# Kernel optimization log

Hardware: AMD Instinct MI355X
Metric: run time of the kernel (lower is better)

## Reference

```python
import jax, jax.numpy as jnp
import numpy as np

HIDDEN = 128
N_LAYERS = 6
N_NODES = 50000
N_EDGES = 640000


def _glorot(key, shape):
    fan_in, fan_out = shape[0], shape[1]
    lim = (6.0 / (fan_in + fan_out)) ** 0.5
    return jax.random.uniform(key, shape, jnp.float32, -lim, lim)


def setup_inputs() -> dict:
    key = jax.random.key(0)
    ks = jax.random.split(key, 8)
    pos = jax.random.normal(ks[0], (N_NODES, 3), jnp.float32)
    edge_attr = jax.random.normal(ks[1], (N_EDGES, 3), jnp.float32)
    edge_index = jax.random.randint(ks[2], (2, N_EDGES), 0, N_NODES, jnp.int64)
    enc_w = _glorot(ks[3], (3, HIDDEN)); enc_b = jnp.zeros((HIDDEN,), jnp.float32)
    dec_w = _glorot(ks[4], (HIDDEN, 3)); dec_b = jnp.zeros((3,), jnp.float32)
    lk = jax.random.split(ks[5], 4 * N_LAYERS)
    edge_w1 = jnp.stack([_glorot(lk[4 * i + 0], (3 * HIDDEN, HIDDEN)) for i in range(N_LAYERS)])
    edge_w2 = jnp.stack([_glorot(lk[4 * i + 1], (HIDDEN, HIDDEN)) for i in range(N_LAYERS)])
    node_w1 = jnp.stack([_glorot(lk[4 * i + 2], (2 * HIDDEN, HIDDEN)) for i in range(N_LAYERS)])
    node_w2 = jnp.stack([_glorot(lk[4 * i + 3], (HIDDEN, HIDDEN)) for i in range(N_LAYERS)])
    edge_b1 = jnp.zeros((N_LAYERS, HIDDEN), jnp.float32)
    edge_b2 = jnp.zeros((N_LAYERS, HIDDEN), jnp.float32)
    node_b1 = jnp.zeros((N_LAYERS, HIDDEN), jnp.float32)
    node_b2 = jnp.zeros((N_LAYERS, HIDDEN), jnp.float32)
    return dict(pos=pos, edge_attr=edge_attr, edge_index=edge_index,
                enc_w=enc_w, enc_b=enc_b, dec_w=dec_w, dec_b=dec_b,
                edge_w1=edge_w1, edge_b1=edge_b1, edge_w2=edge_w2, edge_b2=edge_b2,
                node_w1=node_w1, node_b1=node_b1, node_w2=node_w2, node_b2=node_b2)


def _interaction(x, ef, src, dst, ew1, eb1, ew2, eb2, nw1, nb1, nw2, nb2, n_nodes):
    # message: concat(x_i=x[dst], x_j=x[src], edge_feature) -> edge MLP
    m = jnp.concatenate([x[dst], x[src], ef], axis=-1)            # [E, 3H]
    m = jax.nn.relu(m @ ew1 + eb1) @ ew2 + eb2                     # [E, H]
    # scatter-mean by target node
    sums = jax.ops.segment_sum(m, dst, num_segments=n_nodes)      # [N, H]
    cnt = jax.ops.segment_sum(jnp.ones((m.shape[0],), m.dtype), dst, num_segments=n_nodes)
    aggr = sums / jnp.maximum(cnt, 1.0)[:, None]
    node = jnp.concatenate([x, aggr], axis=-1)                     # [N, 2H]
    node = jax.nn.relu(node @ nw1 + nb1) @ nw2 + nb2               # [N, H]
    return x + node, ef + m


def reference(pos, edge_attr, edge_index, enc_w, enc_b, dec_w, dec_b,
              edge_w1, edge_b1, edge_w2, edge_b2,
              node_w1, node_b1, node_w2, node_b2):
    n_nodes = pos.shape[0]
    src = edge_index[0]
    dst = edge_index[1]
    x = jnp.zeros((n_nodes, HIDDEN), jnp.float32)
    ef = edge_attr @ enc_w + enc_b
    for i in range(N_LAYERS):
        x, ef = _interaction(x, ef, src, dst,
                             edge_w1[i], edge_b1[i], edge_w2[i], edge_b2[i],
                             node_w1[i], node_b1[i], node_w2[i], node_b2[i], n_nodes)
    out = x @ dec_w + dec_b                                        # [N, 3]
    # F.normalize(dim=1, eps=1e-12)
    norm = jnp.linalg.norm(out, axis=1, keepdims=True)
    return out / jnp.maximum(norm, 1e-12)
```

## Files before the change

kernel.cpp:

```cpp
#include <hip/hip_runtime.h>
#include <cstdint>

#define HIDDEN  128
#define NLAYERS 6
#define NNODES  50000
#define NEDGES  640000

typedef short short8 __attribute__((ext_vector_type(8)));
typedef float f32x4  __attribute__((ext_vector_type(4)));
typedef unsigned int   u32x4 __attribute__((ext_vector_type(4)));
typedef unsigned short u16x4 __attribute__((ext_vector_type(4)));

__device__ __forceinline__ float bf2f(unsigned short u) {
    return __uint_as_float(((unsigned int)u) << 16);
}
__device__ __forceinline__ unsigned short f2bf(float f) {
    unsigned int u = __float_as_uint(f);
    unsigned int r = u + 0x7FFFu + ((u >> 16) & 1u);
    return (unsigned short)(r >> 16);
}
__device__ __forceinline__ unsigned int pack2(float a, float b) {
    unsigned int r;
    asm("v_cvt_pk_bf16_f32 %0, %1, %2" : "=v"(r) : "v"(a), "v"(b));
    return r;
}
__device__ __forceinline__ void unpack8u(u32x4 v, float* f) {
    f[0] = bf2f((unsigned short)(v.x & 0xffff)); f[1] = bf2f((unsigned short)(v.x >> 16));
    f[2] = bf2f((unsigned short)(v.y & 0xffff)); f[3] = bf2f((unsigned short)(v.y >> 16));
    f[4] = bf2f((unsigned short)(v.z & 0xffff)); f[5] = bf2f((unsigned short)(v.z >> 16));
    f[6] = bf2f((unsigned short)(v.w & 0xffff)); f[7] = bf2f((unsigned short)(v.w >> 16));
}

__device__ __forceinline__ void barrier_lgkm() {
    asm volatile("s_waitcnt lgkmcnt(0)" ::: "memory");
    __builtin_amdgcn_s_barrier();
    __builtin_amdgcn_sched_barrier(0);
}

__global__ void detect_kernel(const int* __restrict__ ei, int* __restrict__ flag)
{
    int lane = threadIdx.x;
    int v = ei[2 * lane + 1];
    unsigned long long b = __ballot(v != 0);
    if (lane == 0) *flag = (b != 0ULL) ? 1 : 0;
}

__global__ void normidx_kernel(const int* __restrict__ ei, const int* __restrict__ flag,
                               int* __restrict__ s32, int* __restrict__ d32)
{
    int e = blockIdx.x * blockDim.x + threadIdx.x;
    if (e >= NEDGES) return;
    int s, d;
    if (*flag) { s = ei[e]; d = ei[NEDGES + e]; }
    else       { s = ei[2 * e]; d = ei[2 * (NEDGES + e)]; }
    s32[e] = min(max(s, 0), NNODES - 1);
    d32[e] = min(max(d, 0), NNODES - 1);
}

__global__ void degree_kernel(const int* __restrict__ dst, int* __restrict__ deg)
{
    int e = blockIdx.x * blockDim.x + threadIdx.x;
    if (e < NEDGES) atomicAdd(&deg[dst[e]], 1);
}

#define SCAN_T 1024
__global__ void scan_kernel(const int* __restrict__ deg, int* __restrict__ off,
                            int* __restrict__ cursor)
{
    __shared__ int part[SCAN_T];
    const int t = threadIdx.x;
    const int CH = (NNODES + SCAN_T - 1) / SCAN_T;
    const int base = t * CH;
    int s = 0;
    for (int i = 0; i < CH; ++i) {
        int idx = base + i;
        if (idx < NNODES) s += deg[idx];
    }
    part[t] = s;
    __syncthreads();
    for (int d = 1; d < SCAN_T; d <<= 1) {
        int v = (t >= d) ? part[t - d] : 0;
        __syncthreads();
        part[t] += v;
        __syncthreads();
    }
    int run = (t == 0) ? 0 : part[t - 1];
    for (int i = 0; i < CH; ++i) {
        int idx = base + i;
        if (idx < NNODES) {
            off[idx] = run;
            cursor[idx] = run;
            run += deg[idx];
        }
    }
    if (t == SCAN_T - 1) off[NNODES] = run;
}

__global__ void scatter_kernel(const int* __restrict__ s32, const int* __restrict__ d32,
                               int* __restrict__ cursor,
                               int* __restrict__ sp, int* __restrict__ dp, int* __restrict__ ep)
{
    int e = blockIdx.x * blockDim.x + threadIdx.x;
    if (e >= NEDGES) return;
    int d = d32[e];
    int p = atomicAdd(&cursor[d], 1);
    sp[p] = s32[e];
    dp[p] = d;
    ep[p] = e;
}

__global__ void transpose_kernel(const float* __restrict__ W, unsigned short* __restrict__ WT,
                                 int K, int N, int L)
{
    long idx = (long)blockIdx.x * 256 + threadIdx.x;
    long tot = (long)L * K * N;
    if (idx >= tot) return;
    int kn = (int)(idx % ((long)K * N));
    int l  = (int)(idx / ((long)K * N));
    int k = kn / N;
    int n = kn % N;
    WT[(long)l * K * N + (long)n * K + k] = f2bf(W[idx]);
}

__global__ void encode_kernel(const float* __restrict__ ea,
                              const float* __restrict__ w,
                              const float* __restrict__ b,
                              const int* __restrict__ ep,
                              unsigned short* __restrict__ ef)
{
    int idx = blockIdx.x * blockDim.x + threadIdx.x;
    int p = idx >> 5;
    if (p >= NEDGES) return;
    int e = ep[p];
    int j = (idx & 31) << 2;
    float a0 = ea[e * 3 + 0], a1 = ea[e * 3 + 1], a2 = ea[e * 3 + 2];
    float4 w0 = *(const float4*)(w + 0 * HIDDEN + j);
    float4 w1 = *(const float4*)(w + 1 * HIDDEN + j);
    float4 w2 = *(const float4*)(w + 2 * HIDDEN + j);
    float4 bb = *(const float4*)(b + j);
    ushort4 o;
    o.x = f2bf(fmaf(a0, w0.x, fmaf(a1, w1.x, fmaf(a2, w2.x, bb.x))));
    o.y = f2bf(fmaf(a0, w0.y, fmaf(a1, w1.y, fmaf(a2, w2.y, bb.y))));
    o.z = f2bf(fmaf(a0, w0.z, fmaf(a1, w1.z, fmaf(a2, w2.z, bb.z))));
    o.w = f2bf(fmaf(a0, w0.w, fmaf(a1, w1.w, fmaf(a2, w2.w, bb.w))));
    *(ushort4*)(ef + (long)p * HIDDEN + j) = o;
}

__global__ __launch_bounds__(256, 3)
void edge_layer_mfma(const unsigned short* __restrict__ Xa,
                     const unsigned short* __restrict__ Xb,
                     unsigned short* __restrict__ ef,
                     float* __restrict__ sums,
                     const int* __restrict__ sp,
                     const int* __restrict__ dp,
                     const unsigned short* __restrict__ W1T,
                     const float* __restrict__ b1,
                     const unsigned short* __restrict__ W2T,
                     const float* __restrict__ b2)
{
    __shared__ __align__(16) unsigned char buf[45056];
    unsigned short* Hs = (unsigned short*)buf;
    unsigned short* Bs = (unsigned short*)(buf + 34816);
    __shared__ int dv[128];
    __shared__ int sv[128];

    const int tid = threadIdx.x;
    const int nwg = (int)gridDim.x;
    const int bid = (int)blockIdx.x;
    const int sb  = (bid & 7) * (nwg >> 3) + (bid >> 3);
    const long eb = (long)sb * 128;

    if (tid < 128) dv[tid]       = dp[eb + tid];
    else           sv[tid - 128] = sp[eb + tid - 128];

    const int lane = tid & 63;
    const int wv   = tid >> 6;
    const int mn   = lane & 15;
    const int q    = lane >> 4;
    const int bn   = tid >> 1;
    const int bk   = (tid & 1) << 4;

    u32x4 pw0, pw1;
    {
        const unsigned short* wp = W1T + (long)bn * 384 + 256 + bk;
        pw0 = *(const u32x4*)wp;
        pw1 = *(const u32x4*)(wp + 8);
    }

    short8 efold0[4], efold1[4];
    {
        const unsigned short* a0 = ef + (eb + wv * 32 + mn) * HIDDEN + (q << 3);
        const unsigned short* a1 = a0 + 16 * HIDDEN;
#pragma unroll
        for (int c = 0; c < 4; ++c) {
            efold0[c] = *(const short8*)(a0 + (c << 5));
            efold1[c] = *(const short8*)(a1 + (c << 5));
        }
    }

    f32x4 acc[2][8];
#pragma unroll
    for (int h = 0; h < 2; ++h)
#pragma unroll
        for (int t = 0; t < 8; ++t) acc[h][t] = (f32x4)0.0f;

    for (int c = 0; c < 4; ++c) {
        *(u32x4*)&Bs[bn * 40 + bk]     = pw0;
        *(u32x4*)&Bs[bn * 40 + bk + 8] = pw1;
        barrier_lgkm();
        if (c + 1 < 4) {
            const unsigned short* wp = W1T + (long)bn * 384 + 256 + ((c + 1) << 5) + bk;
            pw0 = *(const u32x4*)wp;
            pw1 = *(const u32x4*)(wp + 8);
        }
        short8 af0 = efold0[c];
        short8 af1 = efold1[c];
#pragma unroll
        for (int nt = 0; nt < 8; ++nt) {
            short8 bf = *(short8*)&Bs[(nt * 16 + mn) * 40 + (q << 3)];
            acc[0][nt] = __builtin_amdgcn_mfma_f32_16x16x32_bf16(af0, bf, acc[0][nt], 0, 0, 0);
            acc[1][nt] = __builtin_amdgcn_mfma_f32_16x16x32_bf16(af1, bf, acc[1][nt], 0, 0, 0);
        }
        barrier_lgkm();
    }

#pragma unroll
    for (int h = 0; h < 2; ++h)
#pragma unroll
        for (int nt = 0; nt < 8; ++nt)
#pragma unroll
            for (int r = 0; r < 4; r += 2) {
                unsigned int p = pack2(acc[h][nt][r], acc[h][nt][r + 1]);
                Hs[(wv * 32 + h * 16 + q * 4 + r)     * 136 + nt * 16 + mn] = (unsigned short)p;
                Hs[(wv * 32 + h * 16 + q * 4 + r + 1) * 136 + nt * 16 + mn] = (unsigned short)(p >> 16);
            }

    {
        const int row  = wv * 32 + (lane >> 1);
        const int ch   = (lane & 1) << 6;
        const unsigned short* xap = Xa + (long)dv[row] * HIDDEN + ch;
        const unsigned short* xbp = Xb + (long)sv[row] * HIDDEN + ch;
        unsigned short* hp = &Hs[row * 136 + ch];
#pragma unroll
        for (int i = 0; i < 8; ++i) {
            u32x4 va = *(const u32x4*)(xap + (i << 3));
            u32x4 vb = *(const u32x4*)(xbp + (i << 3));
            u32x4 vp = *(u32x4*)(hp + (i << 3));
            float fa[8], fb[8], fp[8];
            unpack8u(va, fa); unpack8u(vb, fb); unpack8u(vp, fp);
            const float* bp = b1 + ch + (i << 3);
            u32x4 nw;
            float h0 = fmaxf(fp[0] + fa[0] + fb[0] + bp[0], 0.0f);
            float h1 = fmaxf(fp[1] + fa[1] + fb[1] + bp[1], 0.0f);
            float h2 = fmaxf(fp[2] + fa[2] + fb[2] + bp[2], 0.0f);
            float h3 = fmaxf(fp[3] + fa[3] + fb[3] + bp[3], 0.0f);
            float h4 = fmaxf(fp[4] + fa[4] + fb[4] + bp[4], 0.0f);
            float h5 = fmaxf(fp[5] + fa[5] + fb[5] + bp[5], 0.0f);
            float h6 = fmaxf(fp[6] + fa[6] + fb[6] + bp[6], 0.0f);
            float h7 = fmaxf(fp[7] + fa[7] + fb[7] + bp[7], 0.0f);
            nw.x = pack2(h0, h1); nw.y = pack2(h2, h3);
            nw.z = pack2(h4, h5); nw.w = pack2(h6, h7);
            *(u32x4*)(hp + (i << 3)) = nw;
        }
    }

    f32x4 acc2[2][8];
#pragma unroll
    for (int h = 0; h < 2; ++h)
#pragma unroll
        for (int t = 0; t < 8; ++t) acc2[h][t] = (f32x4)0.0f;
    {
        const unsigned short* wp = W2T + (long)bn * 128 + bk;
        pw0 = *(const u32x4*)wp;
        pw1 = *(const u32x4*)(wp + 8);
    }
    for (int c = 0; c < 4; ++c) {
        *(u32x4*)&Bs[bn * 40 + bk]     = pw0;
        *(u32x4*)&Bs[bn * 40 + bk + 8] = pw1;
        barrier_lgkm();
        if (c + 1 < 4) {
            const unsigned short* wp = W2T + (long)bn * 128 + ((c + 1) << 5) + bk;
            pw0 = *(const u32x4*)wp;
            pw1 = *(const u32x4*)(wp + 8);
        }
        short8 af0 = *(short8*)&Hs[(wv * 32 + mn) * 136 + (c << 5) + (q << 3)];
        short8 af1 = *(short8*)&Hs[(wv * 32 + 16 + mn) * 136 + (c << 5) + (q << 3)];
#pragma unroll
        for (int nt = 0; nt < 8; ++nt) {
            short8 bf = *(short8*)&Bs[(nt * 16 + mn) * 40 + (q << 3)];
            acc2[0][nt] = __builtin_amdgcn_mfma_f32_16x16x32_bf16(af0, bf, acc2[0][nt], 0, 0, 0);
            acc2[1][nt] = __builtin_amdgcn_mfma_f32_16x16x32_bf16(af1, bf, acc2[1][nt], 0, 0, 0);
        }
        barrier_lgkm();
    }

#pragma unroll
    for (int h = 0; h < 2; ++h)
#pragma unroll
        for (int nt = 0; nt < 8; ++nt) {
            float b2v = b2[nt * 16 + mn];
#pragma unroll
            for (int r = 0; r < 4; r += 2) {
                unsigned int p = pack2(acc2[h][nt][r] + b2v, acc2[h][nt][r + 1] + b2v);
                Hs[(wv * 32 + h * 16 + q * 4 + r)     * 136 + nt * 16 + mn] = (unsigned short)p;
                Hs[(wv * 32 + h * 16 + q * 4 + r + 1) * 136 + nt * 16 + mn] = (unsigned short)(p >> 16);
            }
        }

#pragma unroll
    for (int h = 0; h < 2; ++h) {
        const int row = wv * 32 + h * 16 + mn;
        unsigned short* ep_ = ef + (eb + row) * HIDDEN + (q << 3);
#pragma unroll
        for (int c = 0; c < 4; ++c) {
            u32x4 mh = *(u32x4*)&Hs[row * 136 + (c << 5) + (q << 3)];
            float m[8], e[8];
            unpack8u(mh, m);
            short8 eo = h ? efold1[c] : efold0[c];
            u32x4 eu = *(u32x4*)&eo;
            unpack8u(eu, e);
            u32x4 nw;
            nw.x = pack2(e[0] + m[0], e[1] + m[1]);
            nw.y = pack2(e[2] + m[2], e[3] + m[3]);
            nw.z = pack2(e[4] + m[4], e[5] + m[5]);
            nw.w = pack2(e[6] + m[6], e[7] + m[7]);
            *(u32x4*)(ep_ + (c << 5)) = nw;
        }
    }

    {
        const int cp = (tid & 63) << 1;
        const int qr = tid >> 6;
        float s0 = 0.0f, s1 = 0.0f;
        int cur = dv[qr * 32];
        for (int r = 0; r < 32; ++r) {
            const int row = qr * 32 + r;
            const int d = dv[row];
            if (d != cur) {
                atomicAdd(&sums[(long)cur * HIDDEN + cp], s0);
                atomicAdd(&sums[(long)cur * HIDDEN + cp + 1], s1);
                s0 = 0.0f; s1 = 0.0f;
                cur = d;
            }
            unsigned int u = *(unsigned int*)&Hs[row * 136 + cp];
            s0 += bf2f((unsigned short)(u & 0xffff));
            s1 += bf2f((unsigned short)(u >> 16));
        }
        atomicAdd(&sums[(long)cur * HIDDEN + cp], s0);
        atomicAdd(&sums[(long)cur * HIDDEN + cp + 1], s1);
    }
}

__global__ __launch_bounds__(256, 5)
void node_layer_mfma(float* __restrict__ x,
                     float* __restrict__ sums,
                     const int* __restrict__ deg,
                     const unsigned short* __restrict__ N1T,
                     const float* __restrict__ b1,
                     const unsigned short* __restrict__ N2T,
                     const float* __restrict__ b2,
                     const unsigned short* __restrict__ W1Tn,
                     unsigned short* __restrict__ Xa,
                     unsigned short* __restrict__ Xb)
{
    __shared__ __align__(16) unsigned char nbuf[27648];
    unsigned short* Hs = (unsigned short*)nbuf;
    unsigned short* Bs = (unsigned short*)(nbuf + 17408);

    const int tid = threadIdx.x;
    const long n0 = (long)blockIdx.x * 64;

    const int lane = tid & 63;
    const int wv   = tid >> 6;
    const int mn   = lane & 15;
    const int q    = lane >> 4;
    const int srow = tid >> 2;
    const int sseg = tid & 3;
    const int bn   = tid >> 1;
    const int bk   = (tid & 1) << 4;

    long arow = n0 + wv * 16 + mn;
    if (arow >= NNODES) arow = NNODES - 1;
    const float* xr = x + arow * HIDDEN;
    const float* sr = sums + arow * HIDDEN;
    const float cv = 1.0f / fmaxf((float)deg[arow], 1.0f);

    f32x4 acc[8];
#pragma unroll
    for (int t = 0; t < 8; ++t) acc[t] = (f32x4)0.0f;

    float4 pa0, pa1;
    u32x4 pb0, pb1;
    {
        const unsigned short* wp = N1T + (long)bn * 256 + bk;
        pb0 = *(const u32x4*)wp;
        pb1 = *(const u32x4*)(wp + 8);
        const float* ap = xr + (q << 3);
        pa0 = *(const float4*)ap;
        pa1 = *(const float4*)(ap + 4);
    }
    float scCur = 1.0f;
    for (int c = 0; c < 8; ++c) {
        short8 af;
        {
            unsigned int* au = (unsigned int*)&af;
            au[0] = pack2(pa0.x * scCur, pa0.y * scCur);
            au[1] = pack2(pa0.z * scCur, pa0.w * scCur);
            au[2] = pack2(pa1.x * scCur, pa1.y * scCur);
            au[3] = pack2(pa1.z * scCur, pa1.w * scCur);
        }
        *(u32x4*)&Bs[bn * 40 + bk]     = pb0;
        *(u32x4*)&Bs[bn * 40 + bk + 8] = pb1;
        barrier_lgkm();
        if (c + 1 < 8) {
            const int cn = c + 1;
            const float* base = (cn < 4) ? xr : sr;
            scCur = (cn < 4) ? 1.0f : cv;
            const float* ap = base + ((cn & 3) << 5) + (q << 3);
            pa0 = *(const float4*)ap;
            pa1 = *(const float4*)(ap + 4);
            const unsigned short* wp = N1T + (long)bn * 256 + (cn << 5) + bk;
            pb0 = *(const u32x4*)wp;
            pb1 = *(const u32x4*)(wp + 8);
        }
#pragma unroll
        for (int nt = 0; nt < 8; ++nt) {
            short8 bf = *(short8*)&Bs[(nt * 16 + mn) * 40 + (q << 3)];
            acc[nt] = __builtin_amdgcn_mfma_f32_16x16x32_bf16(af, bf, acc[nt], 0, 0, 0);
        }
        barrier_lgkm();
    }

    {
        long row = n0 + srow;
        if (row < NNODES) {
            float4 z = make_float4(0.f, 0.f, 0.f, 0.f);
            float* p = sums + row * HIDDEN + (sseg << 5);
#pragma unroll
            for (int i = 0; i < 8; ++i) ((float4*)p)[i] = z;
        }
    }

#pragma unroll
    for (int nt = 0; nt < 8; ++nt) {
        float b1v = b1[nt * 16 + mn];
#pragma unroll
        for (int r = 0; r < 4; r += 2) {
            float h0 = fmaxf(acc[nt][r]     + b1v, 0.0f);
            float h1 = fmaxf(acc[nt][r + 1] + b1v, 0.0f);
            unsigned int p = pack2(h0, h1);
            Hs[(wv * 16 + q * 4 + r)     * 136 + nt * 16 + mn] = (unsigned short)p;
            Hs[(wv * 16 + q * 4 + r + 1) * 136 + nt * 16 + mn] = (unsigned short)(p >> 16);
        }
    }

    f32x4 acc2[8];
#pragma unroll
    for (int t = 0; t < 8; ++t) acc2[t] = (f32x4)0.0f;
    {
        const unsigned short* wp = N2T + (long)bn * 128 + bk;
        pb0 = *(const u32x4*)wp;
        pb1 = *(const u32x4*)(wp + 8);
    }
    for (int c = 0; c < 4; ++c) {
        *(u32x4*)&Bs[bn * 40 + bk]     = pb0;
        *(u32x4*)&Bs[bn * 40 + bk + 8] = pb1;
        barrier_lgkm();
        if (c + 1 < 4) {
            const unsigned short* wp = N2T + (long)bn * 128 + ((c + 1) << 5) + bk;
            pb0 = *(const u32x4*)wp;
            pb1 = *(const u32x4*)(wp + 8);
        }
        short8 af = *(short8*)&Hs[(wv * 16 + mn) * 136 + (c << 5) + (q << 3)];
#pragma unroll
        for (int nt = 0; nt < 8; ++nt) {
            short8 bf = *(short8*)&Bs[(nt * 16 + mn) * 40 + (q << 3)];
            acc2[nt] = __builtin_amdgcn_mfma_f32_16x16x32_bf16(af, bf, acc2[nt], 0, 0, 0);
        }
        barrier_lgkm();
    }

#pragma unroll
    for (int nt = 0; nt < 8; ++nt) {
        float b2v = b2[nt * 16 + mn];
        float xns[4];
#pragma unroll
        for (int r = 0; r < 4; ++r) {
            long row = n0 + wv * 16 + q * 4 + r;
            float xn = 0.0f;
            if (row < NNODES) {
                float* p = x + row * HIDDEN + nt * 16 + mn;
                xn = *p + acc2[nt][r] + b2v;
                *p = xn;
            }
            xns[r] = xn;
        }
        unsigned int p0 = pack2(xns[0], xns[1]);
        unsigned int p1 = pack2(xns[2], xns[3]);
        Hs[(wv * 16 + q * 4 + 0) * 136 + nt * 16 + mn] = (unsigned short)p0;
        Hs[(wv * 16 + q * 4 + 1) * 136 + nt * 16 + mn] = (unsigned short)(p0 >> 16);
        Hs[(wv * 16 + q * 4 + 2) * 136 + nt * 16 + mn] = (unsigned short)p1;
        Hs[(wv * 16 + q * 4 + 3) * 136 + nt * 16 + mn] = (unsigned short)(p1 >> 16);
    }

    if (W1Tn) {
#pragma unroll
        for (int half = 0; half < 2; ++half) {
            f32x4 accN[8];
#pragma unroll
            for (int t = 0; t < 8; ++t) accN[t] = (f32x4)0.0f;
            const int kbase = half << 7;
            {
                const unsigned short* wp = W1Tn + (long)bn * 384 + kbase + bk;
                pb0 = *(const u32x4*)wp;
                pb1 = *(const u32x4*)(wp + 8);
            }
            for (int c = 0; c < 4; ++c) {
                *(u32x4*)&Bs[bn * 40 + bk]     = pb0;
                *(u32x4*)&Bs[bn * 40 + bk + 8] = pb1;
                barrier_lgkm();
                if (c + 1 < 4) {
                    const unsigned short* wp = W1Tn + (long)bn * 384 + kbase + ((c + 1) << 5) + bk;
                    pb0 = *(const u32x4*)wp;
                    pb1 = *(const u32x4*)(wp + 8);
                }
                short8 af = *(short8*)&Hs[(wv * 16 + mn) * 136 + (c << 5) + (q << 3)];
#pragma unroll
                for (int nt = 0; nt < 8; ++nt) {
                    short8 bf = *(short8*)&Bs[(nt * 16 + mn) * 40 + (q << 3)];
                    accN[nt] = __builtin_amdgcn_mfma_f32_16x16x32_bf16(af, bf, accN[nt], 0, 0, 0);
                }
                barrier_lgkm();
            }
            unsigned short* Xout = half ? Xb : Xa;
#pragma unroll
            for (int nt = 0; nt < 8; ++nt) {
#pragma unroll
                for (int r = 0; r < 4; r += 2) {
                    unsigned int p = pack2(accN[nt][r], accN[nt][r + 1]);
                    long row0 = n0 + wv * 16 + q * 4 + r;
                    if (row0 < NNODES)
                        Xout[row0 * HIDDEN + nt * 16 + mn] = (unsigned short)p;
                    if (row0 + 1 < NNODES)
                        Xout[(row0 + 1) * HIDDEN + nt * 16 + mn] = (unsigned short)(p >> 16);
                }
            }
        }
    }
}

__global__ void decode_kernel(const float* __restrict__ x,
                              const float* __restrict__ w,
                              const float* __restrict__ b,
                              float* __restrict__ out)
{
    int gid = blockIdx.x * blockDim.x + threadIdx.x;
    int node = gid >> 6;
    int lane = threadIdx.x & 63;
    if (node >= NNODES) return;
    float a0 = 0.f, a1 = 0.f, a2 = 0.f;
#pragma unroll
    for (int k = lane; k < HIDDEN; k += 64) {
        float xv = x[(long)node * HIDDEN + k];
        a0 = fmaf(xv, w[k * 3 + 0], a0);
        a1 = fmaf(xv, w[k * 3 + 1], a1);
        a2 = fmaf(xv, w[k * 3 + 2], a2);
    }
#pragma unroll
    for (int off = 32; off > 0; off >>= 1) {
        a0 += __shfl_down(a0, off);
        a1 += __shfl_down(a1, off);
        a2 += __shfl_down(a2, off);
    }
    if (lane == 0) {
        a0 += b[0]; a1 += b[1]; a2 += b[2];
        float nrm = sqrtf(a0 * a0 + a1 * a1 + a2 * a2);
        float inv = 1.0f / fmaxf(nrm, 1e-12f);
        out[(long)node * 3 + 0] = a0 * inv;
        out[(long)node * 3 + 1] = a1 * inv;
        out[(long)node * 3 + 2] = a2 * inv;
    }
}

extern "C" void kernel_launch(void* const* d_in, const int* in_sizes, int n_in,
                              void* d_out, int out_size, void* d_ws, size_t ws_size,
                              hipStream_t stream)
{
    const float* edge_attr = (const float*)d_in[1];
    const int*   ei        = (const int*)d_in[2];
    const float* enc_w     = (const float*)d_in[3];
    const float* enc_b     = (const float*)d_in[4];
    const float* dec_w     = (const float*)d_in[5];
    const float* dec_b     = (const float*)d_in[6];
    const float* edge_w1   = (const float*)d_in[7];
    const float* edge_b1   = (const float*)d_in[8];
    const float* edge_w2   = (const float*)d_in[9];
    const float* edge_b2   = (const float*)d_in[10];
    const float* node_w1   = (const float*)d_in[11];
    const float* node_b1   = (const float*)d_in[12];
    const float* node_w2   = (const float*)d_in[13];
    const float* node_b2   = (const float*)d_in[14];

    char* ws = (char*)d_ws;
    unsigned short* ef  = (unsigned short*)(ws);
    float* x      = (float*)(ws + 163840000L);
    float* sums   = (float*)(ws + 189440000L);
    int*   src32  = (int*)  (ws + 215040000L);
    int*   dst32  = (int*)  (ws + 217600000L);
    int*   sp     = (int*)  (ws + 220160000L);
    int*   dp     = (int*)  (ws + 222720000L);
    int*   eperm  = (int*)  (ws + 225280000L);
    int*   deg    = (int*)  (ws + 227840000L);
    int*   off    = (int*)  (ws + 228040704L);
    int*   cursor = (int*)  (ws + 228241408L);
    int*   flag   = (int*)  (ws + 228442112L);
    unsigned short* W1T = (unsigned short*)(ws + 228442176L);
    unsigned short* W2T = (unsigned short*)(ws + 229032000L);
    unsigned short* N1T = (unsigned short*)(ws + 229228608L);
    unsigned short* N2T = (unsigned short*)(ws + 229621824L);
    unsigned short* Xa  = (unsigned short*)(ws + 229818432L);
    unsigned short* Xb  = (unsigned short*)(ws + 242618432L);

    float* out = (float*)d_out;

    hipMemsetAsync(x, 0, (size_t)NNODES * HIDDEN * sizeof(float), stream);
    hipMemsetAsync(sums, 0, (size_t)NNODES * HIDDEN * sizeof(float), stream);
    hipMemsetAsync(deg, 0, 200704, stream);
    hipMemsetAsync(Xa, 0, 25600000, stream);

    detect_kernel<<<1, 64, 0, stream>>>(ei, flag);
    normidx_kernel<<<(NEDGES + 255) / 256, 256, 0, stream>>>(ei, flag, src32, dst32);
    degree_kernel<<<(NEDGES + 255) / 256, 256, 0, stream>>>(dst32, deg);
    scan_kernel<<<1, SCAN_T, 0, stream>>>(deg, off, cursor);
    scatter_kernel<<<(NEDGES + 255) / 256, 256, 0, stream>>>(src32, dst32, cursor, sp, dp, eperm);
    encode_kernel<<<(NEDGES * 32 + 255) / 256, 256, 0, stream>>>(edge_attr, enc_w, enc_b, eperm, ef);

    transpose_kernel<<<(6 * 384 * 128 + 255) / 256, 256, 0, stream>>>(edge_w1, W1T, 384, 128, 6);
    transpose_kernel<<<(6 * 128 * 128 + 255) / 256, 256, 0, stream>>>(edge_w2, W2T, 128, 128, 6);
    transpose_kernel<<<(6 * 256 * 128 + 255) / 256, 256, 0, stream>>>(node_w1, N1T, 256, 128, 6);
    transpose_kernel<<<(6 * 128 * 128 + 255) / 256, 256, 0, stream>>>(node_w2, N2T, 128, 128, 6);

    for (int l = 0; l < NLAYERS; ++l) {
        edge_layer_mfma<<<NEDGES / 128, 256, 0, stream>>>(
            Xa, Xb, ef, sums, sp, dp,
            W1T + (long)l * 384 * 128, edge_b1 + (long)l * HIDDEN,
            W2T + (long)l * 128 * 128, edge_b2 + (long)l * HIDDEN);
        const unsigned short* w1next = (l + 1 < NLAYERS) ? (W1T + (long)(l + 1) * 384 * 128) : nullptr;
        node_layer_mfma<<<(NNODES + 63) / 64, 256, 0, stream>>>(
            x, sums, deg,
            N1T + (long)l * 256 * 128, node_b1 + (long)l * HIDDEN,
            N2T + (long)l * 128 * 128, node_b2 + (long)l * HIDDEN,
            w1next, Xa, Xb);
    }

    decode_kernel<<<(NNODES * 64 + 255) / 256, 256, 0, stream>>>(x, dec_w, dec_b, out);
}
```

Measured before the change: 1.546 ms.

## Split edge-layer work across 8 waves of 16 rows instead of 4 waves of 32

The edge layer kernel now launches 512 threads per block, and each wave handles 16 edge rows instead of 32. Per-thread accumulators are halved, weight staging uses one 16-byte load per thread, and the gather, epilogue and segmented atomic reduction are remapped to match. The aim is to cut register pressure and raise occupancy so there are more waves to hide gather latency. In exchange, the shared weight tile is reused by half as many MFMA rows per wave, and the segmented sums flush atomics more often because each run covers only 16 rows.

```diff
diff --git a/kernel.cpp b/kernel.cpp
--- a/kernel.cpp
+++ b/kernel.cpp
@@ -9,7 +9,6 @@
 typedef short short8 __attribute__((ext_vector_type(8)));
 typedef float f32x4  __attribute__((ext_vector_type(4)));
 typedef unsigned int   u32x4 __attribute__((ext_vector_type(4)));
-typedef unsigned short u16x4 __attribute__((ext_vector_type(4)));
 
 __device__ __forceinline__ float bf2f(unsigned short u) {
     return __uint_as_float(((unsigned int)u) << 16);
@@ -146,7 +145,7 @@
     *(ushort4*)(ef + (long)p * HIDDEN + j) = o;
 }
 
-__global__ __launch_bounds__(256, 3)
+__global__ __launch_bounds__(512, 6)
 void edge_layer_mfma(const unsigned short* __restrict__ Xa,
                      const unsigned short* __restrict__ Xb,
                      unsigned short* __restrict__ ef,
@@ -170,79 +169,66 @@
     const int sb  = (bid & 7) * (nwg >> 3) + (bid >> 3);
     const long eb = (long)sb * 128;
 
-    if (tid < 128) dv[tid]       = dp[eb + tid];
-    else           sv[tid - 128] = sp[eb + tid - 128];
+    if (tid < 128)      dv[tid]       = dp[eb + tid];
+    else if (tid < 256) sv[tid - 128] = sp[eb + tid - 128];
 
     const int lane = tid & 63;
     const int wv   = tid >> 6;
     const int mn   = lane & 15;
     const int q    = lane >> 4;
-    const int bn   = tid >> 1;
-    const int bk   = (tid & 1) << 4;
-
-    u32x4 pw0, pw1;
+    const int bn   = tid >> 2;
+    const int bk   = (tid & 3) << 3;
+
+    u32x4 pw0;
     {
         const unsigned short* wp = W1T + (long)bn * 384 + 256 + bk;
         pw0 = *(const u32x4*)wp;
-        pw1 = *(const u32x4*)(wp + 8);
-    }
-
-    short8 efold0[4], efold1[4];
-    {
-        const unsigned short* a0 = ef + (eb + wv * 32 + mn) * HIDDEN + (q << 3);
-        const unsigned short* a1 = a0 + 16 * HIDDEN;
-#pragma unroll
-        for (int c = 0; c < 4; ++c) {
-            efold0[c] = *(const short8*)(a0 + (c << 5));
-            efold1[c] = *(const short8*)(a1 + (c << 5));
-        }
-    }
-
-    f32x4 acc[2][8];
-#pragma unroll
-    for (int h = 0; h < 2; ++h)
-#pragma unroll
-        for (int t = 0; t < 8; ++t) acc[h][t] = (f32x4)0.0f;
+    }
+
+    short8 efold[4];
+    {
+        const unsigned short* a0 = ef + (eb + wv * 16 + mn) * HIDDEN + (q << 3);
+#pragma unroll
+        for (int c = 0; c < 4; ++c) efold[c] = *(const short8*)(a0 + (c << 5));
+    }
+
+    f32x4 acc[8];
+#pragma unroll
+    for (int t = 0; t < 8; ++t) acc[t] = (f32x4)0.0f;
 
     for (int c = 0; c < 4; ++c) {
-        *(u32x4*)&Bs[bn * 40 + bk]     = pw0;
-        *(u32x4*)&Bs[bn * 40 + bk + 8] = pw1;
+        *(u32x4*)&Bs[bn * 40 + bk] = pw0;
         barrier_lgkm();
         if (c + 1 < 4) {
             const unsigned short* wp = W1T + (long)bn * 384 + 256 + ((c + 1) << 5) + bk;
             pw0 = *(const u32x4*)wp;
-            pw1 = *(const u32x4*)(wp + 8);
-        }
-        short8 af0 = efold0[c];
-        short8 af1 = efold1[c];
+        }
+        short8 af = efold[c];
 #pragma unroll
         for (int nt = 0; nt < 8; ++nt) {
             short8 bf = *(short8*)&Bs[(nt * 16 + mn) * 40 + (q << 3)];
-            acc[0][nt] = __builtin_amdgcn_mfma_f32_16x16x32_bf16(af0, bf, acc[0][nt], 0, 0, 0);
-            acc[1][nt] = __builtin_amdgcn_mfma_f32_16x16x32_bf16(af1, bf, acc[1][nt], 0, 0, 0);
-        }
-        barrier_lgkm();
-    }
-
-#pragma unroll
-    for (int h = 0; h < 2; ++h)
-#pragma unroll
-        for (int nt = 0; nt < 8; ++nt)
-#pragma unroll
-            for (int r = 0; r < 4; r += 2) {
-                unsigned int p = pack2(acc[h][nt][r], acc[h][nt][r + 1]);
-                Hs[(wv * 32 + h * 16 + q * 4 + r)     * 136 + nt * 16 + mn] = (unsigned short)p;
-                Hs[(wv * 32 + h * 16 + q * 4 + r + 1) * 136 + nt * 16 + mn] = (unsigned short)(p >> 16);
-            }
-
-    {
-        const int row  = wv * 32 + (lane >> 1);
-        const int ch   = (lane & 1) << 6;
+            acc[nt] = __builtin_amdgcn_mfma_f32_16x16x32_bf16(af, bf, acc[nt], 0, 0, 0);
+        }
+        barrier_lgkm();
+    }
+
+#pragma unroll
+    for (int nt = 0; nt < 8; ++nt)
+#pragma unroll
+        for (int r = 0; r < 4; r += 2) {
+            unsigned int p = pack2(acc[nt][r], acc[nt][r + 1]);
+            Hs[(wv * 16 + q * 4 + r)     * 136 + nt * 16 + mn] = (unsigned short)p;
+            Hs[(wv * 16 + q * 4 + r + 1) * 136 + nt * 16 + mn] = (unsigned short)(p >> 16);
+        }
+
+    {
+        const int row = wv * 16 + (lane >> 2);
+        const int ch  = (lane & 3) << 5;
         const unsigned short* xap = Xa + (long)dv[row] * HIDDEN + ch;
         const unsigned short* xbp = Xb + (long)sv[row] * HIDDEN + ch;
         unsigned short* hp = &Hs[row * 136 + ch];
 #pragma unroll
-        for (int i = 0; i < 8; ++i) {
+        for (int i = 0; i < 4; ++i) {
             u32x4 va = *(const u32x4*)(xap + (i << 3));
             u32x4 vb = *(const u32x4*)(xbp + (i << 3));
             u32x4 vp = *(u32x4*)(hp + (i << 3));
@@ -264,60 +250,49 @@
         }
     }
 
-    f32x4 acc2[2][8];
-#pragma unroll
-    for (int h = 0; h < 2; ++h)
-#pragma unroll
-        for (int t = 0; t < 8; ++t) acc2[h][t] = (f32x4)0.0f;
+    f32x4 acc2[8];
+#pragma unroll
+    for (int t = 0; t < 8; ++t) acc2[t] = (f32x4)0.0f;
     {
         const unsigned short* wp = W2T + (long)bn * 128 + bk;
         pw0 = *(const u32x4*)wp;
-        pw1 = *(const u32x4*)(wp + 8);
     }
     for (int c = 0; c < 4; ++c) {
-        *(u32x4*)&Bs[bn * 40 + bk]     = pw0;
-        *(u32x4*)&Bs[bn * 40 + bk + 8] = pw1;
+        *(u32x4*)&Bs[bn * 40 + bk] = pw0;
         barrier_lgkm();
         if (c + 1 < 4) {
             const unsigned short* wp = W2T + (long)bn * 128 + ((c + 1) << 5) + bk;
             pw0 = *(const u32x4*)wp;
-            pw1 = *(const u32x4*)(wp + 8);
-        }
-        short8 af0 = *(short8*)&Hs[(wv * 32 + mn) * 136 + (c << 5) + (q << 3)];
-        short8 af1 = *(short8*)&Hs[(wv * 32 + 16 + mn) * 136 + (c << 5) + (q << 3)];
+        }
+        short8 af = *(short8*)&Hs[(wv * 16 + mn) * 136 + (c << 5) + (q << 3)];
 #pragma unroll
         for (int nt = 0; nt < 8; ++nt) {
             short8 bf = *(short8*)&Bs[(nt * 16 + mn) * 40 + (q << 3)];
-            acc2[0][nt] = __builtin_amdgcn_mfma_f32_16x16x32_bf16(af0, bf, acc2[0][nt], 0, 0, 0);
-            acc2[1][nt] = __builtin_amdgcn_mfma_f32_16x16x32_bf16(af1, bf, acc2[1][nt], 0, 0, 0);
-        }
-        barrier_lgkm();
-    }
-
-#pragma unroll
-    for (int h = 0; h < 2; ++h)
-#pragma unroll
-        for (int nt = 0; nt < 8; ++nt) {
-            float b2v = b2[nt * 16 + mn];
-#pragma unroll
-            for (int r = 0; r < 4; r += 2) {
-                unsigned int p = pack2(acc2[h][nt][r] + b2v, acc2[h][nt][r + 1] + b2v);
-                Hs[(wv * 32 + h * 16 + q * 4 + r)     * 136 + nt * 16 + mn] = (unsigned short)p;
-                Hs[(wv * 32 + h * 16 + q * 4 + r + 1) * 136 + nt * 16 + mn] = (unsigned short)(p >> 16);
-            }
-        }
-
-#pragma unroll
-    for (int h = 0; h < 2; ++h) {
-        const int row = wv * 32 + h * 16 + mn;
+            acc2[nt] = __builtin_amdgcn_mfma_f32_16x16x32_bf16(af, bf, acc2[nt], 0, 0, 0);
+        }
+        barrier_lgkm();
+    }
+
+#pragma unroll
+    for (int nt = 0; nt < 8; ++nt) {
+        float b2v = b2[nt * 16 + mn];
+#pragma unroll
+        for (int r = 0; r < 4; r += 2) {
+            unsigned int p = pack2(acc2[nt][r] + b2v, acc2[nt][r + 1] + b2v);
+            Hs[(wv * 16 + q * 4 + r)     * 136 + nt * 16 + mn] = (unsigned short)p;
+            Hs[(wv * 16 + q * 4 + r + 1) * 136 + nt * 16 + mn] = (unsigned short)(p >> 16);
+        }
+    }
+
+    {
+        const int row = wv * 16 + mn;
         unsigned short* ep_ = ef + (eb + row) * HIDDEN + (q << 3);
 #pragma unroll
         for (int c = 0; c < 4; ++c) {
             u32x4 mh = *(u32x4*)&Hs[row * 136 + (c << 5) + (q << 3)];
             float m[8], e[8];
             unpack8u(mh, m);
-            short8 eo = h ? efold1[c] : efold0[c];
-            u32x4 eu = *(u32x4*)&eo;
+            u32x4 eu = *(u32x4*)&efold[c];
             unpack8u(eu, e);
             u32x4 nw;
             nw.x = pack2(e[0] + m[0], e[1] + m[1]);
@@ -329,12 +304,12 @@
     }
 
     {
-        const int cp = (tid & 63) << 1;
-        const int qr = tid >> 6;
+        const int cp = lane << 1;
+        const int qr = wv;
         float s0 = 0.0f, s1 = 0.0f;
-        int cur = dv[qr * 32];
-        for (int r = 0; r < 32; ++r) {
-            const int row = qr * 32 + r;
+        int cur = dv[qr * 16];
+        for (int r = 0; r < 16; ++r) {
+            const int row = qr * 16 + r;
             const int d = dv[row];
             if (d != cur) {
                 atomicAdd(&sums[(long)cur * HIDDEN + cp], s0);
@@ -641,7 +616,7 @@
     transpose_kernel<<<(6 * 128 * 128 + 255) / 256, 256, 0, stream>>>(node_w2, N2T, 128, 128, 6);
 
     for (int l = 0; l < NLAYERS; ++l) {
-        edge_layer_mfma<<<NEDGES / 128, 256, 0, stream>>>(
+        edge_layer_mfma<<<NEDGES / 128, 512, 0, stream>>>(
             Xa, Xb, ef, sums, sp, dp,
             W1T + (long)l * 384 * 128, edge_b1 + (long)l * HIDDEN,
             W2T + (long)l * 128 * 128, edge_b2 + (long)l * HIDDEN);
```

Measured after the change: 1.625 ms. +5.1%, slower.

## Split node-layer GEMM output columns across 8 waves with LDS-staged A tiles

Applied to the files above, without the earlier changes.

The node-layer kernel moves from 256 to 512 threads per block. Each pair of waves now shares a 16-row tile and each wave computes half of the 128 output columns. The concatenated [x, aggr/deg] input is loaded cooperatively with coalesced float4 reads, packed to bf16 and staged in shared memory; inverse degrees are precomputed into shared memory. The aim is more parallelism and fewer accumulators per wave. The cost is more LDS traffic, and the tighter launch bound may force register spilling.

```diff
diff --git a/kernel.cpp b/kernel.cpp
--- a/kernel.cpp
+++ b/kernel.cpp
@@ -9,7 +9,7 @@
 typedef short short8 __attribute__((ext_vector_type(8)));
 typedef float f32x4  __attribute__((ext_vector_type(4)));
 typedef unsigned int   u32x4 __attribute__((ext_vector_type(4)));
-typedef unsigned short u16x4 __attribute__((ext_vector_type(4)));
+typedef unsigned int   u32x2 __attribute__((ext_vector_type(2)));
 
 __device__ __forceinline__ float bf2f(unsigned short u) {
     return __uint_as_float(((unsigned int)u) << 16);
@@ -351,7 +351,7 @@
     }
 }
 
-__global__ __launch_bounds__(256, 5)
+__global__ __launch_bounds__(512, 6)
 void node_layer_mfma(float* __restrict__ x,
                      float* __restrict__ sums,
                      const int* __restrict__ deg,
@@ -364,68 +364,70 @@
                      unsigned short* __restrict__ Xb)
 {
     __shared__ __align__(16) unsigned char nbuf[27648];
+    unsigned short* As = (unsigned short*)nbuf;
     unsigned short* Hs = (unsigned short*)nbuf;
     unsigned short* Bs = (unsigned short*)(nbuf + 17408);
+    __shared__ float cInv[64];
 
     const int tid = threadIdx.x;
     const long n0 = (long)blockIdx.x * 64;
+    if (tid < 64) {
+        long n = n0 + tid;
+        cInv[tid] = (n < NNODES) ? 1.0f / fmaxf((float)deg[n], 1.0f) : 0.0f;
+    }
 
     const int lane = tid & 63;
     const int wv   = tid >> 6;
+    const int wb   = wv & 3;
+    const int nh   = wv >> 2;
     const int mn   = lane & 15;
     const int q    = lane >> 4;
-    const int srow = tid >> 2;
-    const int sseg = tid & 3;
-    const int bn   = tid >> 1;
-    const int bk   = (tid & 1) << 4;
-
-    long arow = n0 + wv * 16 + mn;
-    if (arow >= NNODES) arow = NNODES - 1;
-    const float* xr = x + arow * HIDDEN;
-    const float* sr = sums + arow * HIDDEN;
-    const float cv = 1.0f / fmaxf((float)deg[arow], 1.0f);
-
-    f32x4 acc[8];
-#pragma unroll
-    for (int t = 0; t < 8; ++t) acc[t] = (f32x4)0.0f;
-
-    float4 pa0, pa1;
-    u32x4 pb0, pb1;
-    {
+    const int srow = tid >> 3;
+    const int ss   = tid & 7;
+    const int bn   = tid >> 2;
+    const int bk   = (tid & 3) << 3;
+
+    long nr = n0 + srow;
+    if (nr >= NNODES) nr = NNODES - 1;
+
+    barrier_lgkm();
+
+    f32x4 acc[4];
+#pragma unroll
+    for (int t = 0; t < 4; ++t) acc[t] = (f32x4)0.0f;
+
+    float4 pa;
+    u32x4 pb;
+    {
+        const float* spx = x + nr * HIDDEN + (ss << 2);
+        pa = *(const float4*)spx;
         const unsigned short* wp = N1T + (long)bn * 256 + bk;
-        pb0 = *(const u32x4*)wp;
-        pb1 = *(const u32x4*)(wp + 8);
-        const float* ap = xr + (q << 3);
-        pa0 = *(const float4*)ap;
-        pa1 = *(const float4*)(ap + 4);
+        pb = *(const u32x4*)wp;
     }
     float scCur = 1.0f;
     for (int c = 0; c < 8; ++c) {
-        short8 af;
         {
-            unsigned int* au = (unsigned int*)&af;
-            au[0] = pack2(pa0.x * scCur, pa0.y * scCur);
-            au[1] = pack2(pa0.z * scCur, pa0.w * scCur);
-            au[2] = pack2(pa1.x * scCur, pa1.y * scCur);
-            au[3] = pack2(pa1.z * scCur, pa1.w * scCur);
-        }
-        *(u32x4*)&Bs[bn * 40 + bk]     = pb0;
-        *(u32x4*)&Bs[bn * 40 + bk + 8] = pb1;
+            u32x2 w;
+            w.x = pack2(pa.x * scCur, pa.y * scCur);
+            w.y = pack2(pa.z * scCur, pa.w * scCur);
+            *(u32x2*)&As[srow * 40 + (ss << 2)] = w;
+        }
+        *(u32x4*)&Bs[bn * 40 + bk] = pb;
         barrier_lgkm();
         if (c + 1 < 8) {
             const int cn = c + 1;
-            const float* base = (cn < 4) ? xr : sr;
-            scCur = (cn < 4) ? 1.0f : cv;
-            const float* ap = base + ((cn & 3) << 5) + (q << 3);
-            pa0 = *(const float4*)ap;
-            pa1 = *(const float4*)(ap + 4);
+            const float* base = (cn < 4) ? x : sums;
+            scCur = (cn < 4) ? 1.0f : cInv[srow];
+            const float* spx = base + nr * HIDDEN + ((cn & 3) << 5) + (ss << 2);
+            pa = *(const float4*)spx;
             const unsigned short* wp = N1T + (long)bn * 256 + (cn << 5) + bk;
-            pb0 = *(const u32x4*)wp;
-            pb1 = *(const u32x4*)(wp + 8);
-        }
-#pragma unroll
-        for (int nt = 0; nt < 8; ++nt) {
-            short8 bf = *(short8*)&Bs[(nt * 16 + mn) * 40 + (q << 3)];
+            pb = *(const u32x4*)wp;
+        }
+        short8 af = *(short8*)&As[(wb * 16 + mn) * 40 + (q << 3)];
+#pragma unroll
+        for (int nt = 0; nt < 4; ++nt) {
+            const int ntp = nh * 4 + nt;
+            short8 bf = *(short8*)&Bs[(ntp * 16 + mn) * 40 + (q << 3)];
             acc[nt] = __builtin_amdgcn_mfma_f32_16x16x32_bf16(af, bf, acc[nt], 0, 0, 0);
         }
         barrier_lgkm();
@@ -435,61 +437,61 @@
         long row = n0 + srow;
         if (row < NNODES) {
             float4 z = make_float4(0.f, 0.f, 0.f, 0.f);
-            float* p = sums + row * HIDDEN + (sseg << 5);
-#pragma unroll
-            for (int i = 0; i < 8; ++i) ((float4*)p)[i] = z;
-        }
-    }
-
-#pragma unroll
-    for (int nt = 0; nt < 8; ++nt) {
-        float b1v = b1[nt * 16 + mn];
+            float* p = sums + row * HIDDEN + (ss << 4);
+#pragma unroll
+            for (int i = 0; i < 4; ++i) ((float4*)p)[i] = z;
+        }
+    }
+
+#pragma unroll
+    for (int nt = 0; nt < 4; ++nt) {
+        const int ntp = nh * 4 + nt;
+        float b1v = b1[ntp * 16 + mn];
 #pragma unroll
         for (int r = 0; r < 4; r += 2) {
             float h0 = fmaxf(acc[nt][r]     + b1v, 0.0f);
             float h1 = fmaxf(acc[nt][r + 1] + b1v, 0.0f);
             unsigned int p = pack2(h0, h1);
-            Hs[(wv * 16 + q * 4 + r)     * 136 + nt * 16 + mn] = (unsigned short)p;
-            Hs[(wv * 16 + q * 4 + r + 1) * 136 + nt * 16 + mn] = (unsigned short)(p >> 16);
-        }
-    }
-
-    f32x4 acc2[8];
-#pragma unroll
-    for (int t = 0; t < 8; ++t) acc2[t] = (f32x4)0.0f;
+            Hs[(wb * 16 + q * 4 + r)     * 136 + ntp * 16 + mn] = (unsigned short)p;
+            Hs[(wb * 16 + q * 4 + r + 1) * 136 + ntp * 16 + mn] = (unsigned short)(p >> 16);
+        }
+    }
+
+    f32x4 acc2[4];
+#pragma unroll
+    for (int t = 0; t < 4; ++t) acc2[t] = (f32x4)0.0f;
     {
         const unsigned short* wp = N2T + (long)bn * 128 + bk;
-        pb0 = *(const u32x4*)wp;
-        pb1 = *(const u32x4*)(wp + 8);
+        pb = *(const u32x4*)wp;
     }
     for (int c = 0; c < 4; ++c) {
-        *(u32x4*)&Bs[bn * 40 + bk]     = pb0;
-        *(u32x4*)&Bs[bn * 40 + bk + 8] = pb1;
+        *(u32x4*)&Bs[bn * 40 + bk] = pb;
         barrier_lgkm();
         if (c + 1 < 4) {
             const unsigned short* wp = N2T + (long)bn * 128 + ((c + 1) << 5) + bk;
-            pb0 = *(const u32x4*)wp;
-            pb1 = *(const u32x4*)(wp + 8);
-        }
-        short8 af = *(short8*)&Hs[(wv * 16 + mn) * 136 + (c << 5) + (q << 3)];
-#pragma unroll
-        for (int nt = 0; nt < 8; ++nt) {
-            short8 bf = *(short8*)&Bs[(nt * 16 + mn) * 40 + (q << 3)];
+            pb = *(const u32x4*)wp;
+        }
+        short8 af = *(short8*)&Hs[(wb * 16 + mn) * 136 + (c << 5) + (q << 3)];
+#pragma unroll
+        for (int nt = 0; nt < 4; ++nt) {
+            const int ntp = nh * 4 + nt;
+            short8 bf = *(short8*)&Bs[(ntp * 16 + mn) * 40 + (q << 3)];
             acc2[nt] = __builtin_amdgcn_mfma_f32_16x16x32_bf16(af, bf, acc2[nt], 0, 0, 0);
         }
         barrier_lgkm();
     }
 
 #pragma unroll
-    for (int nt = 0; nt < 8; ++nt) {
-        float b2v = b2[nt * 16 + mn];
+    for (int nt = 0; nt < 4; ++nt) {
+        const int ntp = nh * 4 + nt;
+        float b2v = b2[ntp * 16 + mn];
         float xns[4];
 #pragma unroll
         for (int r = 0; r < 4; ++r) {
-            long row = n0 + wv * 16 + q * 4 + r;
+            long row = n0 + wb * 16 + q * 4 + r;
             float xn = 0.0f;
             if (row < NNODES) {
-                float* p = x + row * HIDDEN + nt * 16 + mn;
+                float* p = x + row * HIDDEN + ntp * 16 + mn;
                 xn = *p + acc2[nt][r] + b2v;
                 *p = xn;
             }
@@ -497,52 +499,51 @@
         }
         unsigned int p0 = pack2(xns[0], xns[1]);
         unsigned int p1 = pack2(xns[2], xns[3]);
-        Hs[(wv * 16 + q * 4 + 0) * 136 + nt * 16 + mn] = (unsigned short)p0;
-        Hs[(wv * 16 + q * 4 + 1) * 136 + nt * 16 + mn] = (unsigned short)(p0 >> 16);
-        Hs[(wv * 16 + q * 4 + 2) * 136 + nt * 16 + mn] = (unsigned short)p1;
-        Hs[(wv * 16 + q * 4 + 3) * 136 + nt * 16 + mn] = (unsigned short)(p1 >> 16);
+        Hs[(wb * 16 + q * 4 + 0) * 136 + ntp * 16 + mn] = (unsigned short)p0;
+        Hs[(wb * 16 + q * 4 + 1) * 136 + ntp * 16 + mn] = (unsigned short)(p0 >> 16);
+        Hs[(wb * 16 + q * 4 + 2) * 136 + ntp * 16 + mn] = (unsigned short)p1;
+        Hs[(wb * 16 + q * 4 + 3) * 136 + ntp * 16 + mn] = (unsigned short)(p1 >> 16);
     }
 
     if (W1Tn) {
 #pragma unroll
         for (int half = 0; half < 2; ++half) {
-            f32x4 accN[8];
-#pragma unroll
-            for (int t = 0; t < 8; ++t) accN[t] = (f32x4)0.0f;
+            f32x4 accN[4];
+#pragma unroll
+            for (int t = 0; t < 4; ++t) accN[t] = (f32x4)0.0f;
             const int kbase = half << 7;
             {
                 const unsigned short* wp = W1Tn + (long)bn * 384 + kbase + bk;
-                pb0 = *(const u32x4*)wp;
-                pb1 = *(const u32x4*)(wp + 8);
+                pb = *(const u32x4*)wp;
             }
             for (int c = 0; c < 4; ++c) {
-                *(u32x4*)&Bs[bn * 40 + bk]     = pb0;
-                *(u32x4*)&Bs[bn * 40 + bk + 8] = pb1;
+                *(u32x4*)&Bs[bn * 40 + bk] = pb;
                 barrier_lgkm();
                 if (c + 1 < 4) {
                     const unsigned short* wp = W1Tn + (long)bn * 384 + kbase + ((c + 1) << 5) + bk;
-                    pb0 = *(const u32x4*)wp;
-                    pb1 = *(const u32x4*)(wp + 8);
+                    pb = *(const u32x4*)wp;
                 }
-                short8 af = *(short8*)&Hs[(wv * 16 + mn) * 136 + (c << 5) + (q << 3)];
-#pragma unroll
-                for (int nt = 0; nt < 8; ++nt) {
-                    short8 bf = *(short8*)&Bs[(nt * 16 + mn) * 40 + (q << 3)];
+                short8 af = *(short8*)&Hs[(wb * 16 + mn) * 136 + (c << 5) + (q << 3)];
+#pragma unroll
+                for (int nt = 0; nt < 4; ++nt) {
+                    const int ntp = nh * 4 + nt;
+                    short8 bf = *(short8*)&Bs[(ntp * 16 + mn) * 40 + (q << 3)];
                     accN[nt] = __builtin_amdgcn_mfma_f32_16x16x32_bf16(af, bf, accN[nt], 0, 0, 0);
                 }
                 barrier_lgkm();
             }
             unsigned short* Xout = half ? Xb : Xa;
 #pragma unroll
-            for (int nt = 0; nt < 8; ++nt) {
+            for (int nt = 0; nt < 4; ++nt) {
+                const int ntp = nh * 4 + nt;
 #pragma unroll
                 for (int r = 0; r < 4; r += 2) {
                     unsigned int p = pack2(accN[nt][r], accN[nt][r + 1]);
-                    long row0 = n0 + wv * 16 + q * 4 + r;
+                    long row0 = n0 + wb * 16 + q * 4 + r;
                     if (row0 < NNODES)
-                        Xout[row0 * HIDDEN + nt * 16 + mn] = (unsigned short)p;
+                        Xout[row0 * HIDDEN + ntp * 16 + mn] = (unsigned short)p;
                     if (row0 + 1 < NNODES)
-                        Xout[(row0 + 1) * HIDDEN + nt * 16 + mn] = (unsigned short)(p >> 16);
+                        Xout[(row0 + 1) * HIDDEN + ntp * 16 + mn] = (unsigned short)(p >> 16);
                 }
             }
         }
@@ -646,7 +647,7 @@
             W1T + (long)l * 384 * 128, edge_b1 + (long)l * HIDDEN,
             W2T + (long)l * 128 * 128, edge_b2 + (long)l * HIDDEN);
         const unsigned short* w1next = (l + 1 < NLAYERS) ? (W1T + (long)(l + 1) * 384 * 128) : nullptr;
-        node_layer_mfma<<<(NNODES + 63) / 64, 256, 0, stream>>>(
+        node_layer_mfma<<<(NNODES + 63) / 64, 512, 0, stream>>>(
             x, sums, deg,
             N1T + (long)l * 256 * 128, node_b1 + (long)l * HIDDEN,
             N2T + (long)l * 128 * 128, node_b2 + (long)l * HIDDEN,
```

After: 1.499 ms. 1.03x faster.
